# Kernel optimization log

Hardware: AMD Instinct MI355X
Metric: run time of the kernel (lower is better)

Reference implementation:

```python
import jax, jax.numpy as jnp
import numpy as np

# Quantization constants (from init_kwargs)
INPUT_SCALE = 0.05
OUTPUT_SCALE = 0.1
OUTPUT_ZERO_POINT = 0
FEATURE_BITWIDTH = 8
Q_MIN = -(1 << (FEATURE_BITWIDTH - 1))       # -128
Q_MAX = (1 << (FEATURE_BITWIDTH - 1)) - 1    #  127

B, IN_F, OUT_F = 8192, 4096, 4096


def setup_inputs() -> dict:
    key = jax.random.key(0)
    k_x, k_w, k_b, k_s = jax.random.split(key, 4)
    # int8 quantized activations and weights
    x = jax.random.randint(k_x, (B, IN_F), Q_MIN, Q_MAX + 1, dtype=jnp.int8)
    weight = jax.random.randint(k_w, (OUT_F, IN_F), Q_MIN, Q_MAX + 1, dtype=jnp.int8)
    # shifted quantized bias (int32)
    bias = jax.random.randint(k_b, (OUT_F,), -1000, 1000, dtype=jnp.int32)
    # per-output-channel weight scale (positive floats)
    weight_scale = jax.random.uniform(k_s, (OUT_F,), dtype=jnp.float32, minval=0.001, maxval=0.01)
    return {"x": x, "weight": weight, "bias": bias, "weight_scale": weight_scale}


def reference(x, weight, bias, weight_scale):
    # int32-accumulated GEMM: [B, in] @ [in, out] + bias -> [B, out]
    acc = jnp.matmul(x.astype(jnp.int32), weight.astype(jnp.int32).T,
                     preferred_element_type=jnp.int32) + bias[None, :]
    # dequant/requant epilogue with per-channel scale
    out = acc.astype(jnp.float32) * (INPUT_SCALE * weight_scale[None, :] / OUTPUT_SCALE) + OUTPUT_ZERO_POINT
    out = jnp.clip(jnp.round(out), Q_MIN, Q_MAX).astype(jnp.int8)
    return out
```

## Files before the change

### kernel.cpp

```cpp
#include <hip/hip_runtime.h>
#include <cstdint>
#include <cstddef>

#define M_DIM 8192
#define N_DIM 4096
#define K_DIM 4096

#define BM 256
#define BN 256

using i32x4 = __attribute__((ext_vector_type(4))) int;

__device__ __forceinline__ void async_load16(const void* g, void* l) {
    __builtin_amdgcn_global_load_lds(
        (const __attribute__((address_space(1))) void*)g,
        (__attribute__((address_space(3))) void*)l,
        16, 0, 0);
}

__global__ __launch_bounds__(256) void pack_i8_kernel(const int4* __restrict__ xsrc,
                                                      int* __restrict__ xdst,
                                                      const int4* __restrict__ wsrc,
                                                      int* __restrict__ wdst,
                                                      int nxblocks) {
    const bool isw = (int)blockIdx.x >= nxblocks;
    const int4* src = isw ? wsrc : xsrc;
    int*       dst  = isw ? wdst : xdst;
    const long bb   = isw ? ((long)blockIdx.x - nxblocks) : (long)blockIdx.x;
    const long base = bb * 1024 + threadIdx.x;
#pragma unroll
    for (int j = 0; j < 4; ++j) {
        const long i = base + 256 * j;
        const int4 v = src[i];
        dst[i] = (v.x & 0xff) | ((v.y & 0xff) << 8) | ((v.z & 0xff) << 16) | (v.w << 24);
    }
}

__global__ __launch_bounds__(512, 2) void qgemm_i8_kernel(const int8_t* __restrict__ A,
                                                          const int8_t* __restrict__ B,
                                                          const int* __restrict__ bias,
                                                          const float* __restrict__ wscale,
                                                          int* __restrict__ C) {
    __shared__ int8_t LDS[131072];

    const int tid  = threadIdx.x;
    const int wave = tid >> 6;
    const int lane = tid & 63;
    const int wm = wave >> 2;
    const int wn = wave & 3;

    const int lin = (int)(blockIdx.y * 16 + blockIdx.x);
    const int swz = (lin & 7) * 64 + (lin >> 3);
    const int bm = swz >> 4;
    const int bn = swz & 15;

    const int8_t* Ab = A + (size_t)bm * BM * K_DIM;
    const int8_t* Bb = B + (size_t)bn * BN * K_DIM;

    const int l8 = lane >> 3;
    const int l7 = lane & 7;
    const int8_t* Ag = Ab + (size_t)(wave * 16 + l8) * K_DIM + ((l7 ^ l8) * 16);
    const int8_t* Bg = Bb + (size_t)(wave * 16 + l8) * K_DIM + ((l7 ^ l8) * 16);
    const int sdst = wave * 2048;

    const int l15 = lane & 15;
    const int qh  = lane >> 4;
    const int a_off0 = wm * 8192 + l15 * 128 + ((qh ^ l7) * 16);
    const int a_off1 = a_off0 ^ 64;
    const int b_off0 = 65536 + wn * 4096 + l15 * 128 + ((qh ^ l7) * 16);
    const int b_off1 = b_off0 ^ 64;

    i32x4 acc[4][4][2] = {};
    i32x4 af[4][2];
    i32x4 bf[2][2][2];

#define ISSUE_HT(GB, REG, BUF, HH, T) do { \
    async_load16((GB) + (size_t)((HH) * 128)     * K_DIM + (size_t)(T) * 128, \
                 &LDS[(REG) + (BUF) * 32768 + (HH) * 16384 + sdst]); \
    async_load16((GB) + (size_t)((HH) * 128 + 8) * K_DIM + (size_t)(T) * 128, \
                 &LDS[(REG) + (BUF) * 32768 + (HH) * 16384 + sdst + 1024]); \
} while (0)

#define LOAD_AF(BUF, MH) do { \
    _Pragma("unroll") \
    for (int mi = 0; mi < 4; ++mi) { \
        af[mi][0] = *(const i32x4*)&LDS[a_off0 + (BUF) * 32768 + (MH) * 16384 + mi * 2048]; \
        af[mi][1] = *(const i32x4*)&LDS[a_off1 + (BUF) * 32768 + (MH) * 16384 + mi * 2048]; \
    } \
} while (0)

#define LOAD_BF(BUF, NH) do { \
    _Pragma("unroll") \
    for (int ni = 0; ni < 2; ++ni) { \
        bf[NH][ni][0] = *(const i32x4*)&LDS[b_off0 + (BUF) * 32768 + (NH) * 16384 + ni * 2048]; \
        bf[NH][ni][1] = *(const i32x4*)&LDS[b_off1 + (BUF) * 32768 + (NH) * 16384 + ni * 2048]; \
    } \
} while (0)

#define VM6 asm volatile("s_waitcnt vmcnt(6)" ::: "memory")
#define VM0 asm volatile("s_waitcnt vmcnt(0)" ::: "memory")

#define PHASE(LOADS, QD, NHB, ISSUES, CHK) do { \
    LOADS; \
    ISSUES; \
    CHK; \
    __builtin_amdgcn_s_barrier(); \
    __builtin_amdgcn_s_setprio(1); \
    _Pragma("unroll") \
    for (int mi = 0; mi < 4; ++mi) { \
        _Pragma("unroll") \
        for (int ni = 0; ni < 2; ++ni) { \
            acc[QD][mi][ni] = __builtin_amdgcn_mfma_i32_16x16x64_i8(af[mi][0], bf[NHB][ni][0], acc[QD][mi][ni], 0, 0, 0); \
            acc[QD][mi][ni] = __builtin_amdgcn_mfma_i32_16x16x64_i8(af[mi][1], bf[NHB][ni][1], acc[QD][mi][ni], 0, 0, 0); \
        } \
    } \
    __builtin_amdgcn_s_setprio(0); \
} while (0)

    ISSUE_HT(Ag, 0,     0, 0, 0);
    ISSUE_HT(Bg, 65536, 0, 0, 0);
    ISSUE_HT(Bg, 65536, 0, 1, 0);
    ISSUE_HT(Ag, 0,     0, 1, 0);
    ISSUE_HT(Ag, 0,     1, 0, 1);
    ISSUE_HT(Bg, 65536, 1, 0, 1);
    ISSUE_HT(Bg, 65536, 1, 1, 1);
    VM6;
    __builtin_amdgcn_s_barrier();

    for (int i = 0; i < 16; ++i) {
        const int V = 2 * i + 1;
        const int W = 2 * i + 2;
        const int X = 2 * i + 3;
        const bool more = (i < 15);

        PHASE({ LOAD_AF(0, 0); LOAD_BF(0, 0); }, 0, 0,
              { ISSUE_HT(Ag, 0,     1, 1, V); }, {});
        PHASE({ LOAD_BF(0, 1); }, 1, 1,
              {}, {});
        PHASE({ LOAD_AF(0, 1); }, 2, 1,
              { if (more) { ISSUE_HT(Ag, 0, 0, 0, W); ISSUE_HT(Bg, 65536, 0, 0, W); } }, {});
        PHASE({}, 3, 0,
              { if (more) ISSUE_HT(Bg, 65536, 0, 1, W); },
              { if (more) { VM6; } else { VM0; } });
        PHASE({ LOAD_AF(1, 0); LOAD_BF(1, 0); }, 0, 0,
              { if (more) ISSUE_HT(Ag, 0,     0, 1, W); }, {});
        PHASE({ LOAD_BF(1, 1); }, 1, 1,
              {}, {});
        PHASE({ LOAD_AF(1, 1); }, 2, 1,
              { if (more) { ISSUE_HT(Ag, 0, 1, 0, X); ISSUE_HT(Bg, 65536, 1, 0, X); } }, {});
        PHASE({}, 3, 0,
              { if (more) ISSUE_HT(Bg, 65536, 1, 1, X); },
              { if (more) { VM6; } });
    }

#undef PHASE
#undef VM0
#undef VM6
#undef LOAD_BF
#undef LOAD_AF
#undef ISSUE_HT

    const int col16 = lane & 15;
    const int rquad = (lane >> 4) * 4;
#pragma unroll
    for (int qd = 0; qd < 4; ++qd) {
        const int mh = qd >> 1;
        const int nh = (qd >> 1) ^ (qd & 1);
#pragma unroll
        for (int ni = 0; ni < 2; ++ni) {
            const int col = bn * BN + nh * 128 + wn * 32 + ni * 16 + col16;
            float s = 0.05f * wscale[col];
            s = s / 0.1f;
            const float bz = (float)bias[col];
#pragma unroll
            for (int mi = 0; mi < 4; ++mi) {
                const int row0 = bm * BM + mh * 128 + wm * 64 + mi * 16 + rquad;
#pragma unroll
                for (int r = 0; r < 4; ++r) {
                    float v = ((float)acc[qd][mi][ni][r] + bz) * s;
                    v = rintf(v);
                    v = fminf(fmaxf(v, -128.0f), 127.0f);
                    C[(size_t)(row0 + r) * N_DIM + col] = (int)v;
                }
            }
        }
    }
}

extern "C" void kernel_launch(void* const* d_in, const int* in_sizes, int n_in,
                              void* d_out, int out_size, void* d_ws, size_t ws_size,
                              hipStream_t stream) {
    const int*   x32    = (const int*)d_in[0];
    const int*   w32    = (const int*)d_in[1];
    const int*   bias   = (const int*)d_in[2];
    const float* wscale = (const float*)d_in[3];
    int*         out    = (int*)d_out;

    int8_t* xp = (int8_t*)d_ws;
    int8_t* wp = xp + (size_t)M_DIM * K_DIM;

    {
        const int nxblocks = (int)((long)M_DIM * K_DIM / 4 / 1024);
        const int nwblocks = (int)((long)N_DIM * K_DIM / 4 / 1024);
        pack_i8_kernel<<<nxblocks + nwblocks, 256, 0, stream>>>(
            (const int4*)x32, (int*)xp, (const int4*)w32, (int*)wp, nxblocks);
    }

    dim3 grid(N_DIM / BN, M_DIM / BM);
    qgemm_i8_kernel<<<grid, 512, 0, stream>>>(xp, wp, bias, wscale, out);
}
```

Baseline: 375.6 us.

## Switch int8 GEMM to 32x32x32 MFMA with reswizzled LDS fragment loads

Replaces the 16x16x64 int8 MFMA tiling with 32x32x32 MFMA instructions, which changes the per-wave accumulator layout, the LDS fragment read pattern and XOR swizzle, and the epilogue row/column mapping. It also moves one B-fragment LDS load to just after the barrier of the preceding phase, and uses a shared scalar base plus per-lane offset for the async global loads. The larger MFMA reads fewer LDS fragments per FLOP and issues fewer instructions. The risks are LDS bank conflicts under the new swizzle, higher register pressure from the 16-wide accumulators, and an epilogue store pattern that may coalesce less well.

New measurement: 402.9 us. 1.07x slower.

```diff
diff --git a/kernel.cpp b/kernel.cpp
--- a/kernel.cpp
+++ b/kernel.cpp
@@ -9,7 +9,8 @@
 #define BM 256
 #define BN 256
 
-using i32x4 = __attribute__((ext_vector_type(4))) int;
+using i32x4  = __attribute__((ext_vector_type(4))) int;
+using i32x16 = __attribute__((ext_vector_type(16))) int;
 
 __device__ __forceinline__ void async_load16(const void* g, void* l) {
     __builtin_amdgcn_global_load_lds(
@@ -59,71 +60,69 @@
 
     const int l8 = lane >> 3;
     const int l7 = lane & 7;
-    const int8_t* Ag = Ab + (size_t)(wave * 16 + l8) * K_DIM + ((l7 ^ l8) * 16);
-    const int8_t* Bg = Bb + (size_t)(wave * 16 + l8) * K_DIM + ((l7 ^ l8) * 16);
+    const int voffS = (wave * 16 + l8) * K_DIM + ((l7 ^ l8) * 16);
     const int sdst = wave * 2048;
 
-    const int l15 = lane & 15;
-    const int qh  = lane >> 4;
-    const int a_off0 = wm * 8192 + l15 * 128 + ((qh ^ l7) * 16);
-    const int a_off1 = a_off0 ^ 64;
-    const int b_off0 = 65536 + wn * 4096 + l15 * 128 + ((qh ^ l7) * 16);
-    const int b_off1 = b_off0 ^ 64;
-
-    i32x4 acc[4][4][2] = {};
-    i32x4 af[4][2];
-    i32x4 bf[2][2][2];
-
-#define ISSUE_HT(GB, REG, BUF, HH, T) do { \
-    async_load16((GB) + (size_t)((HH) * 128)     * K_DIM + (size_t)(T) * 128, \
+    const int l31 = lane & 31;
+    const int l5  = lane >> 5;
+    const int h2  = l7 >> 1;
+    const int aoff = wm * 8192 + l31 * 128 + 16 * (l5 ^ (lane & 1));
+    const int boff = 65536 + wn * 4096 + l31 * 128 + 16 * (l5 ^ (lane & 1));
+
+    i32x16 acc[4][2] = {};
+    i32x4 af[2][4];
+    i32x4 bf[2][4];
+
+#define ISSUE_HT(MATB, REG, BUF, HH, T) do { \
+    const int8_t* _b = (MATB) + (size_t)((HH) * 128) * K_DIM + (size_t)(T) * 128; \
+    async_load16(_b + voffS, \
                  &LDS[(REG) + (BUF) * 32768 + (HH) * 16384 + sdst]); \
-    async_load16((GB) + (size_t)((HH) * 128 + 8) * K_DIM + (size_t)(T) * 128, \
+    async_load16(_b + 8 * K_DIM + voffS, \
                  &LDS[(REG) + (BUF) * 32768 + (HH) * 16384 + sdst + 1024]); \
 } while (0)
 
 #define LOAD_AF(BUF, MH) do { \
     _Pragma("unroll") \
-    for (int mi = 0; mi < 4; ++mi) { \
-        af[mi][0] = *(const i32x4*)&LDS[a_off0 + (BUF) * 32768 + (MH) * 16384 + mi * 2048]; \
-        af[mi][1] = *(const i32x4*)&LDS[a_off1 + (BUF) * 32768 + (MH) * 16384 + mi * 2048]; \
+    for (int mb = 0; mb < 2; ++mb) { \
+        _Pragma("unroll") \
+        for (int kb = 0; kb < 4; ++kb) \
+            af[mb][kb] = *(const i32x4*)&LDS[aoff + (BUF) * 32768 + (MH) * 16384 \
+                                             + mb * 4096 + ((kb ^ h2) * 32)]; \
     } \
 } while (0)
 
 #define LOAD_BF(BUF, NH) do { \
     _Pragma("unroll") \
-    for (int ni = 0; ni < 2; ++ni) { \
-        bf[NH][ni][0] = *(const i32x4*)&LDS[b_off0 + (BUF) * 32768 + (NH) * 16384 + ni * 2048]; \
-        bf[NH][ni][1] = *(const i32x4*)&LDS[b_off1 + (BUF) * 32768 + (NH) * 16384 + ni * 2048]; \
-    } \
+    for (int kb = 0; kb < 4; ++kb) \
+        bf[NH][kb] = *(const i32x4*)&LDS[boff + (BUF) * 32768 + (NH) * 16384 \
+                                         + ((kb ^ h2) * 32)]; \
 } while (0)
 
 #define VM6 asm volatile("s_waitcnt vmcnt(6)" ::: "memory")
 #define VM0 asm volatile("s_waitcnt vmcnt(0)" ::: "memory")
 
-#define PHASE(LOADS, QD, NHB, ISSUES, CHK) do { \
+#define PHASE(LOADS, QD, NHB, ISSUES, CHK, POST) do { \
     LOADS; \
     ISSUES; \
     CHK; \
     __builtin_amdgcn_s_barrier(); \
+    POST; \
     __builtin_amdgcn_s_setprio(1); \
     _Pragma("unroll") \
-    for (int mi = 0; mi < 4; ++mi) { \
-        _Pragma("unroll") \
-        for (int ni = 0; ni < 2; ++ni) { \
-            acc[QD][mi][ni] = __builtin_amdgcn_mfma_i32_16x16x64_i8(af[mi][0], bf[NHB][ni][0], acc[QD][mi][ni], 0, 0, 0); \
-            acc[QD][mi][ni] = __builtin_amdgcn_mfma_i32_16x16x64_i8(af[mi][1], bf[NHB][ni][1], acc[QD][mi][ni], 0, 0, 0); \
-        } \
+    for (int kb = 0; kb < 4; ++kb) { \
+        acc[QD][0] = __builtin_amdgcn_mfma_i32_32x32x32_i8(af[0][kb], bf[NHB][kb], acc[QD][0], 0, 0, 0); \
+        acc[QD][1] = __builtin_amdgcn_mfma_i32_32x32x32_i8(af[1][kb], bf[NHB][kb], acc[QD][1], 0, 0, 0); \
     } \
     __builtin_amdgcn_s_setprio(0); \
 } while (0)
 
-    ISSUE_HT(Ag, 0,     0, 0, 0);
-    ISSUE_HT(Bg, 65536, 0, 0, 0);
-    ISSUE_HT(Bg, 65536, 0, 1, 0);
-    ISSUE_HT(Ag, 0,     0, 1, 0);
-    ISSUE_HT(Ag, 0,     1, 0, 1);
-    ISSUE_HT(Bg, 65536, 1, 0, 1);
-    ISSUE_HT(Bg, 65536, 1, 1, 1);
+    ISSUE_HT(Ab, 0,     0, 0, 0);
+    ISSUE_HT(Bb, 65536, 0, 0, 0);
+    ISSUE_HT(Bb, 65536, 0, 1, 0);
+    ISSUE_HT(Ab, 0,     0, 1, 0);
+    ISSUE_HT(Ab, 0,     1, 0, 1);
+    ISSUE_HT(Bb, 65536, 1, 0, 1);
+    ISSUE_HT(Bb, 65536, 1, 1, 1);
     VM6;
     __builtin_amdgcn_s_barrier();
 
@@ -134,23 +133,25 @@
         const bool more = (i < 15);
 
         PHASE({ LOAD_AF(0, 0); LOAD_BF(0, 0); }, 0, 0,
-              { ISSUE_HT(Ag, 0,     1, 1, V); }, {});
-        PHASE({ LOAD_BF(0, 1); }, 1, 1,
-              {}, {});
+              { ISSUE_HT(Ab, 0,     1, 1, V); }, {},
+              { LOAD_BF(0, 1); });
+        PHASE({}, 1, 1,
+              {}, {}, {});
         PHASE({ LOAD_AF(0, 1); }, 2, 1,
-              { if (more) { ISSUE_HT(Ag, 0, 0, 0, W); ISSUE_HT(Bg, 65536, 0, 0, W); } }, {});
+              { if (more) { ISSUE_HT(Ab, 0, 0, 0, W); ISSUE_HT(Bb, 65536, 0, 0, W); } }, {}, {});
         PHASE({}, 3, 0,
-              { if (more) ISSUE_HT(Bg, 65536, 0, 1, W); },
-              { if (more) { VM6; } else { VM0; } });
+              { if (more) ISSUE_HT(Bb, 65536, 0, 1, W); },
+              { if (more) { VM6; } else { VM0; } }, {});
         PHASE({ LOAD_AF(1, 0); LOAD_BF(1, 0); }, 0, 0,
-              { if (more) ISSUE_HT(Ag, 0,     0, 1, W); }, {});
-        PHASE({ LOAD_BF(1, 1); }, 1, 1,
-              {}, {});
+              { if (more) ISSUE_HT(Ab, 0,     0, 1, W); }, {},
+              { LOAD_BF(1, 1); });
+        PHASE({}, 1, 1,
+              {}, {}, {});
         PHASE({ LOAD_AF(1, 1); }, 2, 1,
-              { if (more) { ISSUE_HT(Ag, 0, 1, 0, X); ISSUE_HT(Bg, 65536, 1, 0, X); } }, {});
+              { if (more) { ISSUE_HT(Ab, 0, 1, 0, X); ISSUE_HT(Bb, 65536, 1, 0, X); } }, {}, {});
         PHASE({}, 3, 0,
-              { if (more) ISSUE_HT(Bg, 65536, 1, 1, X); },
-              { if (more) { VM6; } });
+              { if (more) ISSUE_HT(Bb, 65536, 1, 1, X); },
+              { if (more) { VM6; } }, {});
     }
 
 #undef PHASE
@@ -160,28 +161,24 @@
 #undef LOAD_AF
 #undef ISSUE_HT
 
-    const int col16 = lane & 15;
-    const int rquad = (lane >> 4) * 4;
 #pragma unroll
     for (int qd = 0; qd < 4; ++qd) {
         const int mh = qd >> 1;
         const int nh = (qd >> 1) ^ (qd & 1);
-#pragma unroll
-        for (int ni = 0; ni < 2; ++ni) {
-            const int col = bn * BN + nh * 128 + wn * 32 + ni * 16 + col16;
-            float s = 0.05f * wscale[col];
-            s = s / 0.1f;
-            const float bz = (float)bias[col];
-#pragma unroll
-            for (int mi = 0; mi < 4; ++mi) {
-                const int row0 = bm * BM + mh * 128 + wm * 64 + mi * 16 + rquad;
-#pragma unroll
-                for (int r = 0; r < 4; ++r) {
-                    float v = ((float)acc[qd][mi][ni][r] + bz) * s;
-                    v = rintf(v);
-                    v = fminf(fmaxf(v, -128.0f), 127.0f);
-                    C[(size_t)(row0 + r) * N_DIM + col] = (int)v;
-                }
+        const int col = bn * BN + nh * 128 + wn * 32 + l31;
+        float s = 0.05f * wscale[col];
+        s = s / 0.1f;
+        const float bz = (float)bias[col];
+#pragma unroll
+        for (int mb = 0; mb < 2; ++mb) {
+            const int row0 = bm * BM + mh * 128 + wm * 64 + mb * 32 + 4 * l5;
+#pragma unroll
+            for (int r = 0; r < 16; ++r) {
+                const int row = row0 + (r & 3) + 8 * (r >> 2);
+                float v = ((float)acc[qd][mb][r] + bz) * s;
+                v = rintf(v);
+                v = fminf(fmaxf(v, -128.0f), 127.0f);
+                C[(size_t)row * N_DIM + col] = (int)v;
             }
         }
     }
```
